# Optimization experiments

Measured on AMD Instinct MI355X. Metric: run time of the kernel, lower is better.

The kernel has to match this reference:

```python
import jax, jax.numpy as jnp
import numpy as np

N = 8192          # number of latent vectors z
M = 16384         # number of KDE sample points (multiple of N_EMB)
N_EMB = 16        # n_embeddings on the circle
Z_DIM = 2         # fixed by get_embeddings (cos/sin stack)
INIT_LOG_SIGMA = 0.0


def setup_inputs() -> dict:
    key = jax.random.key(0)
    k1, k2 = jax.random.split(key)
    z = jax.random.normal(k1, (N, Z_DIM), dtype=jnp.float32)
    eps = jax.random.normal(k2, (M // N_EMB, Z_DIM), dtype=jnp.float32)
    # get_embeddings: points on a circle of radius 4
    angles = jnp.linspace(0.0, 2.0 * np.pi, N_EMB)
    embeddings = (jnp.stack([jnp.cos(angles), jnp.sin(angles)], axis=1) * 4.0).astype(jnp.float32)
    log_sigma = jnp.full((1,), INIT_LOG_SIGMA, dtype=jnp.float32)
    temperature = jnp.full((1,), 0.5, dtype=jnp.float32)
    return {"z": z, "embeddings": embeddings, "log_sigma": log_sigma,
            "eps": eps, "temperature": temperature}


def reference(z, embeddings, log_sigma, eps, temperature):
    T = temperature[0]
    ls = log_sigma[0]
    sigma = jnp.exp(ls)
    z_dim = z.shape[1]
    n = z.shape[0]
    # mean: (n_emb, D); samples e: (n_emb * M//n_emb, D) == (M, D)
    mean = (1.0 - T) * embeddings
    e = (mean[:, None, :] + eps[None, :, :] * T).reshape(-1, z_dim)
    # squared euclidean distance (N, M) via gemm expansion (same math as ||z-e||^2)
    d = (jnp.sum(z * z, axis=1)[:, None]
         + jnp.sum(e * e, axis=1)[None, :]
         - 2.0 * (z @ e.T))
    alpha = -1.0 / (2.0 * sigma ** 2)
    lse = jax.nn.logsumexp(alpha * d, axis=0)  # reduce over N -> (M,)
    # np.log(np.e) == 1.0
    loss = (-jnp.mean(lse)
            + 0.5 * z_dim * (2.0 * ls - 1.0)
            + jnp.log(jnp.float32(n)))
    return loss
```

## Files before the change

kernel.cpp:

```cpp
#include <hip/hip_runtime.h>
#include <math.h>

#define N_TOT 8192
#define M_TOT 16384
#define EPS_N 1024
#define N_EMB 16

#define LOG2E 1.4426950408889634f
#define LN2   0.6931471805599453f
#define EXP2(x) __builtin_amdgcn_exp2f(x)
#define LOG2F_(x) __builtin_amdgcn_logf(x)

#define BLOCK 256
#define IC    128
#define NICH  (N_TOT / IC)
#define LCH   128
#define NLCH  (EPS_N / LCH)

__global__ __launch_bounds__(BLOCK) void gemm_partial_kernel(
    const float* __restrict__ z, const float* __restrict__ emb,
    const float* __restrict__ log_sigma, const float* __restrict__ eps,
    const float* __restrict__ temperature, float* __restrict__ part)
{
    __shared__ float4 rows[IC * 5];
    __shared__ float red[4][N_EMB * LCH];

    const int t  = threadIdx.x;
    const int l0 = blockIdx.x * LCH;
    const int ib = blockIdx.y;

    const float ls = log_sigma[0];
    const float T  = temperature[0];
    const float alpha = -0.5f * EXP2(LOG2E * (-2.0f * ls));
    const float La  = LOG2E * alpha;
    const float omT = 1.0f - T;

    {
        const int il = t & (IC - 1);
        const int kh = t >> 7;
        const int i  = ib * IC + il;
        const float z0 = z[2 * i], z1 = z[2 * i + 1];
        const float c  = La * (z0 * z0 + z1 * z1);
        const float b0 = -2.0f * La * z0, b1 = -2.0f * La * z1;
        float4 pa, pb;
#pragma unroll
        for (int kk = 0; kk < 4; ++kk) {
            int k = kh * 8 + kk;
            float m0 = omT * emb[2 * k], m1 = omT * emb[2 * k + 1];
            ((float*)&pa)[kk] = EXP2(c + b0 * m0 + b1 * m1);
        }
#pragma unroll
        for (int kk = 0; kk < 4; ++kk) {
            int k = kh * 8 + 4 + kk;
            float m0 = omT * emb[2 * k], m1 = omT * emb[2 * k + 1];
            ((float*)&pb)[kk] = EXP2(c + b0 * m0 + b1 * m1);
        }
        rows[il * 5 + kh * 2]     = pa;
        rows[il * 5 + kh * 2 + 1] = pb;
        if (kh == 0)
            rows[il * 5 + 4] = make_float4(T * b0, T * b1, 0.0f, 0.0f);
    }

    const int lane = t & 63;
    const int w    = t >> 6;
    const float2* eps2 = (const float2*)eps;
    const float2 ua = eps2[l0 + lane];
    const float2 ub = eps2[l0 + 64 + lane];

    __syncthreads();

    float sa[N_EMB] = {0.0f};
    float sb[N_EMB] = {0.0f};
#pragma unroll 2
    for (int n = 0; n < IC / 4; ++n) {
        const int ir = w * (IC / 4) + n;
        float4 p0 = rows[ir * 5 + 0];
        float4 p1 = rows[ir * 5 + 1];
        float4 p2 = rows[ir * 5 + 2];
        float4 p3 = rows[ir * 5 + 3];
        float4 tb = rows[ir * 5 + 4];
        float qa = EXP2(fmaf(tb.y, ua.y, tb.x * ua.x));
        float qb = EXP2(fmaf(tb.y, ub.y, tb.x * ub.x));
        float pk[16];
        *(float4*)&pk[0]  = p0; *(float4*)&pk[4]  = p1;
        *(float4*)&pk[8]  = p2; *(float4*)&pk[12] = p3;
#pragma unroll
        for (int k = 0; k < N_EMB; ++k) {
            sa[k] = fmaf(pk[k], qa, sa[k]);
            sb[k] = fmaf(pk[k], qb, sb[k]);
        }
    }

#pragma unroll
    for (int k = 0; k < N_EMB; ++k) {
        red[w][k * LCH + lane]      = sa[k];
        red[w][k * LCH + 64 + lane] = sb[k];
    }
    __syncthreads();
#pragma unroll
    for (int r = 0; r < (N_EMB * LCH) / BLOCK; ++r) {
        const int e  = t + r * BLOCK;
        const float S = red[0][e] + red[1][e] + red[2][e] + red[3][e];
        const int k  = e >> 7;
        const int lc = e & (LCH - 1);
        part[ib * M_TOT + k * EPS_N + l0 + lc] = S;
    }
}

__global__ __launch_bounds__(BLOCK) void reduce_kernel(
    const float* __restrict__ emb, const float* __restrict__ log_sigma,
    const float* __restrict__ eps, const float* __restrict__ temperature,
    const float* __restrict__ part, float* __restrict__ bsum)
{
    const int j = blockIdx.x * BLOCK + threadIdx.x;
    const float ls = log_sigma[0];
    const float T  = temperature[0];
    const float alpha = -0.5f * EXP2(LOG2E * (-2.0f * ls));

    float S = 0.0f;
#pragma unroll 8
    for (int ib = 0; ib < NICH; ++ib)
        S += part[ib * M_TOT + j];

    const int k = j >> 10, l = j & (EPS_N - 1);
    const float omT = 1.0f - T;
    const float e0 = omT * emb[2 * k]     + T * eps[2 * l];
    const float e1 = omT * emb[2 * k + 1] + T * eps[2 * l + 1];
    const float g  = LOG2E * alpha * (e0 * e0 + e1 * e1);

    float v = g + LOG2F_(S);

#pragma unroll
    for (int off = 32; off; off >>= 1) v += __shfl_down(v, off, 64);
    __shared__ float wsum[BLOCK / 64];
    const int lane = threadIdx.x & 63, w = threadIdx.x >> 6;
    if (lane == 0) wsum[w] = v;
    __syncthreads();
    if (threadIdx.x == 0)
        bsum[blockIdx.x] = wsum[0] + wsum[1] + wsum[2] + wsum[3];
}

__global__ void final_kernel(const float* __restrict__ log_sigma,
                             const float* __restrict__ bsum,
                             float* __restrict__ out)
{
    float v = bsum[threadIdx.x];
#pragma unroll
    for (int off = 32; off; off >>= 1) v += __shfl_down(v, off, 64);
    if (threadIdx.x == 0) {
        const float ls = log_sigma[0];
        const float sum_lse = v * LN2;
        out[0] = -sum_lse / (float)M_TOT + (2.0f * ls - 1.0f) + 9.010913347279288f;
    }
}

extern "C" void kernel_launch(void* const* d_in, const int* in_sizes, int n_in,
                              void* d_out, int out_size, void* d_ws, size_t ws_size,
                              hipStream_t stream)
{
    const float* z    = (const float*)d_in[0];
    const float* emb  = (const float*)d_in[1];
    const float* lsig = (const float*)d_in[2];
    const float* eps  = (const float*)d_in[3];
    const float* temp = (const float*)d_in[4];

    float* part = (float*)d_ws;
    float* bsum = part + (size_t)NICH * M_TOT;

    dim3 grid1(NLCH, NICH);
    gemm_partial_kernel<<<grid1, BLOCK, 0, stream>>>(z, emb, lsig, eps, temp, part);
    reduce_kernel<<<M_TOT / BLOCK, BLOCK, 0, stream>>>(emb, lsig, eps, temp, part, bsum);
    final_kernel<<<1, 64, 0, stream>>>(lsig, bsum, (float*)d_out);
}
```

Measured before the change: 73.99 us.

## Fuse partial GEMM, column reduction and final sum via atomic last-block counters

Merges the three kernels into one. Each column chunk's last-arriving block, detected through an atomic counter, reduces the partials for that chunk. A second counter lets the last chunk write the final loss. This removes two kernel launches and their gaps, but adds a memset launch, fences and a tail where only 8 blocks do the full column reduction serially.

Result: slower. 104.0 us (+40.6%).

```diff
diff --git a/kernel.cpp b/kernel.cpp
--- a/kernel.cpp
+++ b/kernel.cpp
@@ -17,16 +17,23 @@
 #define LCH   128
 #define NLCH  (EPS_N / LCH)
 
-__global__ __launch_bounds__(BLOCK) void gemm_partial_kernel(
+__global__ __launch_bounds__(BLOCK) void fused_kernel(
     const float* __restrict__ z, const float* __restrict__ emb,
     const float* __restrict__ log_sigma, const float* __restrict__ eps,
-    const float* __restrict__ temperature, float* __restrict__ part)
+    const float* __restrict__ temperature,
+    float* __restrict__ part,
+    float* __restrict__ colsum,
+    unsigned int* __restrict__ cnt,
+    float* __restrict__ out)
 {
     __shared__ float4 rows[IC * 5];
     __shared__ float red[4][N_EMB * LCH];
+    __shared__ float wsum[4];
+    __shared__ unsigned int sflag;
 
     const int t  = threadIdx.x;
-    const int l0 = blockIdx.x * LCH;
+    const int lc = blockIdx.x;
+    const int l0 = lc * LCH;
     const int ib = blockIdx.y;
 
     const float ls = log_sigma[0];
@@ -102,55 +109,53 @@
         const int e  = t + r * BLOCK;
         const float S = red[0][e] + red[1][e] + red[2][e] + red[3][e];
         const int k  = e >> 7;
-        const int lc = e & (LCH - 1);
-        part[ib * M_TOT + k * EPS_N + l0 + lc] = S;
+        const int lcl = e & (LCH - 1);
+        part[ib * M_TOT + k * EPS_N + l0 + lcl] = S;
     }
-}
 
-__global__ __launch_bounds__(BLOCK) void reduce_kernel(
-    const float* __restrict__ emb, const float* __restrict__ log_sigma,
-    const float* __restrict__ eps, const float* __restrict__ temperature,
-    const float* __restrict__ part, float* __restrict__ bsum)
-{
-    const int j = blockIdx.x * BLOCK + threadIdx.x;
-    const float ls = log_sigma[0];
-    const float T  = temperature[0];
-    const float alpha = -0.5f * EXP2(LOG2E * (-2.0f * ls));
+    __syncthreads();
+    if (t == 0) {
+        __threadfence();
+        unsigned int old = atomicAdd(&cnt[lc], 1u);
+        sflag = (old == (unsigned int)(NICH - 1)) ? 1u : 0u;
+    }
+    __syncthreads();
+    if (sflag == 0u) return;
 
-    float S = 0.0f;
+    __threadfence();
+    float vsum = 0.0f;
+#pragma unroll
+    for (int r = 0; r < (N_EMB * LCH) / BLOCK; ++r) {
+        const int e  = t + r * BLOCK;
+        const int k  = e >> 7;
+        const int ll = e & (LCH - 1);
+        const int j  = k * EPS_N + l0 + ll;
+        float S = 0.0f;
 #pragma unroll 8
-    for (int ib = 0; ib < NICH; ++ib)
-        S += part[ib * M_TOT + j];
+        for (int ic = 0; ic < NICH; ++ic)
+            S += part[ic * M_TOT + j];
+        const float e0 = omT * emb[2 * k]     + T * eps[2 * (l0 + ll)];
+        const float e1 = omT * emb[2 * k + 1] + T * eps[2 * (l0 + ll) + 1];
+        const float g  = La * (e0 * e0 + e1 * e1);
+        vsum += g + LOG2F_(S);
+    }
+#pragma unroll
+    for (int off = 32; off; off >>= 1) vsum += __shfl_down(vsum, off, 64);
+    if (lane == 0) wsum[w] = vsum;
+    __syncthreads();
 
-    const int k = j >> 10, l = j & (EPS_N - 1);
-    const float omT = 1.0f - T;
-    const float e0 = omT * emb[2 * k]     + T * eps[2 * l];
-    const float e1 = omT * emb[2 * k + 1] + T * eps[2 * l + 1];
-    const float g  = LOG2E * alpha * (e0 * e0 + e1 * e1);
-
-    float v = g + LOG2F_(S);
-
+    if (t == 0) {
+        colsum[lc] = wsum[0] + wsum[1] + wsum[2] + wsum[3];
+        __threadfence();
+        unsigned int o2 = atomicAdd(&cnt[NLCH], 1u);
+        if (o2 == (unsigned int)(NLCH - 1)) {
+            __threadfence();
+            float v = 0.0f;
 #pragma unroll
-    for (int off = 32; off; off >>= 1) v += __shfl_down(v, off, 64);
-    __shared__ float wsum[BLOCK / 64];
-    const int lane = threadIdx.x & 63, w = threadIdx.x >> 6;
-    if (lane == 0) wsum[w] = v;
-    __syncthreads();
-    if (threadIdx.x == 0)
-        bsum[blockIdx.x] = wsum[0] + wsum[1] + wsum[2] + wsum[3];
-}
-
-__global__ void final_kernel(const float* __restrict__ log_sigma,
-                             const float* __restrict__ bsum,
-                             float* __restrict__ out)
-{
-    float v = bsum[threadIdx.x];
-#pragma unroll
-    for (int off = 32; off; off >>= 1) v += __shfl_down(v, off, 64);
-    if (threadIdx.x == 0) {
-        const float ls = log_sigma[0];
-        const float sum_lse = v * LN2;
-        out[0] = -sum_lse / (float)M_TOT + (2.0f * ls - 1.0f) + 9.010913347279288f;
+            for (int c = 0; c < NLCH; ++c) v += colsum[c];
+            const float sum_lse = v * LN2;
+            out[0] = -sum_lse / (float)M_TOT + (2.0f * ls - 1.0f) + 9.010913347279288f;
+        }
     }
 }
 
@@ -164,11 +169,13 @@
     const float* eps  = (const float*)d_in[3];
     const float* temp = (const float*)d_in[4];
 
-    float* part = (float*)d_ws;
-    float* bsum = part + (size_t)NICH * M_TOT;
+    unsigned int* cnt = (unsigned int*)d_ws;
+    float* part   = (float*)d_ws + 64;
+    float* colsum = part + (size_t)NICH * M_TOT;
+
+    hipMemsetAsync(d_ws, 0, 64, stream);
 
     dim3 grid1(NLCH, NICH);
-    gemm_partial_kernel<<<grid1, BLOCK, 0, stream>>>(z, emb, lsig, eps, temp, part);
-    reduce_kernel<<<M_TOT / BLOCK, BLOCK, 0, stream>>>(emb, lsig, eps, temp, part, bsum);
-    final_kernel<<<1, 64, 0, stream>>>(lsig, bsum, (float*)d_out);
+    fused_kernel<<<grid1, BLOCK, 0, stream>>>(z, emb, lsig, eps, temp,
+                                              part, colsum, cnt, (float*)d_out);
 }
```
